# Kernel tuning notes

Hardware: AMD Instinct MI355X
Metric: run time of the kernel (lower is better)

Reference implementation:

```python
import jax, jax.numpy as jnp
import numpy as np

NEG_SLOPE = 0.2
LN_EPS = 1e-5


def _gat_layer(x, src, dst, W, a_src, a_dst, N):
    # x: [N, Fin], W: [Fin, H*C], a_src/a_dst: [H, C]
    H, C = a_src.shape
    h = (x @ W).reshape(N, H, C)
    al_src = (h * a_src).sum(-1)  # [N, H]
    al_dst = (h * a_dst).sum(-1)  # [N, H]
    e = jax.nn.leaky_relu(al_src[src] + al_dst[dst], NEG_SLOPE)  # [E, H]
    m = jax.ops.segment_max(e, dst, num_segments=N)
    e = jnp.exp(e - m[dst])
    denom = jax.ops.segment_sum(e, dst, num_segments=N)
    alpha = e / denom[dst]  # softmax over incoming edges per dst node
    msg = h[src] * alpha[:, :, None]  # [E, H, C]
    return jax.ops.segment_sum(msg, dst, num_segments=N)  # [N, H, C]


def _layer_norm(x, g, b):
    mu = x.mean(-1, keepdims=True)
    var = ((x - mu) ** 2).mean(-1, keepdims=True)
    return (x - mu) * jax.lax.rsqrt(var + LN_EPS) * g + b


def setup_inputs() -> dict:
    key = jax.random.key(0)
    ks = jax.random.split(key, 20)
    N, E, Fin, Ch, H = 50000, 800000, 128, 64, 4
    s = lambda k, shp, sc=0.05: jax.random.normal(k, shp, dtype=jnp.float32) * sc
    return {
        "x": jax.random.normal(ks[0], (N, Fin), dtype=jnp.float32),
        "edge_index": jax.random.randint(ks[1], (2, E), 0, N, dtype=jnp.int64),
        "W1": s(ks[2], (Fin, H * Ch)),
        "att_src1": s(ks[3], (H, Ch)),
        "att_dst1": s(ks[4], (H, Ch)),
        "b1": jnp.zeros((H * Ch,), jnp.float32),
        "ln1_g": jnp.ones((H * Ch,), jnp.float32),
        "ln1_b": jnp.zeros((H * Ch,), jnp.float32),
        "W2": s(ks[5], (H * Ch, Ch)),
        "att_src2": s(ks[6], (1, Ch)),
        "att_dst2": s(ks[7], (1, Ch)),
        "b2": jnp.zeros((Ch,), jnp.float32),
        "ln2_g": jnp.ones((Ch,), jnp.float32),
        "ln2_b": jnp.zeros((Ch,), jnp.float32),
        "fc1_W": s(ks[8], (Ch, Ch // 2)),
        "fc1_b": jnp.zeros((Ch // 2,), jnp.float32),
        "fc2_W": s(ks[9], (Ch // 2, 1)),
        "fc2_b": jnp.zeros((1,), jnp.float32),
    }


def reference(x, edge_index, W1, att_src1, att_dst1, b1, ln1_g, ln1_b,
              W2, att_src2, att_dst2, b2, ln2_g, ln2_b,
              fc1_W, fc1_b, fc2_W, fc2_b):
    N = x.shape[0]
    # PyG GATConv adds self-loops by default
    loop = jnp.arange(N, dtype=edge_index.dtype)
    src = jnp.concatenate([edge_index[0], loop])
    dst = jnp.concatenate([edge_index[1], loop])

    # GAT layer 1 (heads=4, concat) + LayerNorm + ReLU (dropout is identity in eval)
    h = _gat_layer(x, src, dst, W1, att_src1, att_dst1, N).reshape(N, -1) + b1
    h = jax.nn.relu(_layer_norm(h, ln1_g, ln1_b))

    # GAT layer 2 (heads=1) + LayerNorm + ReLU
    h = _gat_layer(h, src, dst, W2, att_src2, att_dst2, N).reshape(N, -1) + b2
    h = jax.nn.relu(_layer_norm(h, ln2_g, ln2_b))

    # MLP head
    h = jax.nn.relu(h @ fc1_W + fc1_b)
    return h @ fc2_W + fc2_b  # [N, 1]
```

## Files before the change

### kernel.cpp

```cpp
#include <hip/hip_runtime.h>
#include <hip/hip_fp16.h>
#include <math.h>

#define NEG_SLOPE 0.2f
#define LN_EPS 1e-5f

typedef __attribute__((ext_vector_type(8))) _Float16 half8;
typedef __attribute__((ext_vector_type(4))) _Float16 half4;
typedef __attribute__((ext_vector_type(4))) float floatx4;

static __device__ __forceinline__ float lrelu(float e) {
    return e > 0.0f ? e : NEG_SLOPE * e;
}

__global__ void k_zero(int* __restrict__ p, int n) {
    int i = blockIdx.x * blockDim.x + threadIdx.x;
    if (i < n) p[i] = 0;
}


__global__ __launch_bounds__(256) void k_bcount(
    const int* __restrict__ ei, int* __restrict__ gcount, int E, int N, int NB)
{
    __shared__ int hist[512];
    const int Et = E + N;
    for (int t = threadIdx.x; t < NB; t += 256) hist[t] = 0;
    __syncthreads();
    const int i0 = blockIdx.x * 8192;
#pragma unroll 4
    for (int j = 0; j < 32; ++j) {
        int i = i0 + j * 256 + threadIdx.x;
        if (i < Et) {
            int d = (i < E) ? ei[E + i] : (i - E);
            atomicAdd(&hist[d >> 7], 1);
        }
    }
    __syncthreads();
    for (int t = threadIdx.x; t < NB; t += 256)
        if (hist[t]) atomicAdd(&gcount[t], hist[t]);
}

__global__ __launch_bounds__(512) void k_bscan(
    const int* __restrict__ gcount, int* __restrict__ gbase, int* __restrict__ gcursor,
    int* __restrict__ offs, int NB, int N, int Et)
{
    __shared__ int ws[8];
    const int t = threadIdx.x, lane = t & 63, w = t >> 6;
    int v = (t < NB) ? gcount[t] : 0;
    int x = v;
#pragma unroll
    for (int o = 1; o < 64; o <<= 1) { int u = __shfl_up(x, o); if (lane >= o) x += u; }
    if (lane == 63) ws[w] = x;
    __syncthreads();
    if (t < 8) {
        int y = ws[t];
#pragma unroll
        for (int o = 1; o < 8; o <<= 1) { int u = __shfl_up(y, o); if (t >= o) y += u; }
        ws[t] = y;
    }
    __syncthreads();
    int excl = x - v + (w ? ws[w - 1] : 0);
    if (t < NB) { gbase[t] = excl; gcursor[t] = excl; }
    if (t == 0) offs[N] = Et;
}

__global__ __launch_bounds__(256) void k_bscatter(
    const int* __restrict__ ei, int* __restrict__ gcursor, int2* __restrict__ staged,
    int E, int N, int NB)
{
    __shared__ int hist[512];
    __shared__ int lbase[512];
    const int Et = E + N;
    for (int t = threadIdx.x; t < NB; t += 256) hist[t] = 0;
    __syncthreads();
    const int i0 = blockIdx.x * 8192;
#pragma unroll 4
    for (int j = 0; j < 32; ++j) {
        int i = i0 + j * 256 + threadIdx.x;
        if (i < Et) {
            int d = (i < E) ? ei[E + i] : (i - E);
            atomicAdd(&hist[d >> 7], 1);
        }
    }
    __syncthreads();
    for (int t = threadIdx.x; t < NB; t += 256) {
        int c = hist[t];
        lbase[t] = c ? atomicAdd(&gcursor[t], c) : 0;
    }
    __syncthreads();
    for (int t = threadIdx.x; t < NB; t += 256) hist[t] = 0;
    __syncthreads();
#pragma unroll 4
    for (int j = 0; j < 32; ++j) {
        int i = i0 + j * 256 + threadIdx.x;
        if (i < Et) {
            int s, d;
            if (i < E) { s = ei[i]; d = ei[E + i]; } else { s = d = i - E; }
            int b = d >> 7;
            int k = atomicAdd(&hist[b], 1);
            staged[lbase[b] + k] = make_int2(s, d);
        }
    }
}

__global__ __launch_bounds__(256) void k_bbuild(
    const int2* __restrict__ staged, const int* __restrict__ gcount, const int* __restrict__ gbase,
    int* __restrict__ offs, int* __restrict__ eidx, int N)
{
    __shared__ int ncnt[128];
    __shared__ int lcur[128];
    const int b = blockIdx.x;
    const int node0 = b << 7;
    const int base = gbase[b], cnt = gcount[b];
    for (int t = threadIdx.x; t < 128; t += 256) ncnt[t] = 0;
    __syncthreads();
    for (int t = threadIdx.x; t < cnt; t += 256)
        atomicAdd(&ncnt[staged[base + t].y - node0], 1);
    __syncthreads();
    if (threadIdx.x < 64) {
        const int lane = threadIdx.x;
        int a0 = ncnt[lane], a1 = ncnt[64 + lane];
        int x0 = a0, x1 = a1;
#pragma unroll
        for (int o = 1; o < 64; o <<= 1) {
            int t0 = __shfl_up(x0, o), t1 = __shfl_up(x1, o);
            if (lane >= o) { x0 += t0; x1 += t1; }
        }
        int tot0 = __shfl(x0, 63);
        int e0 = base + x0 - a0;
        int e1 = base + x1 - a1 + tot0;
        lcur[lane] = e0; lcur[64 + lane] = e1;
        int na = node0 + lane, nb = node0 + 64 + lane;
        if (na < N) offs[na] = e0;
        if (nb < N) offs[nb] = e1;
    }
    __syncthreads();
    for (int t = threadIdx.x; t < cnt; t += 256) {
        int2 sd = staged[base + t];
        int pos = atomicAdd(&lcur[sd.y - node0], 1);
        eidx[pos] = sd.x;
    }
}

__global__ __launch_bounds__(256) void k_gemm1(
    const float* __restrict__ x, const float* __restrict__ W1,
    const float* __restrict__ as1, const float* __restrict__ ad1,
    _Float16* __restrict__ h1, float* __restrict__ als, float* __restrict__ ald, int N)
{
    const int lane = threadIdx.x & 63, w = threadIdx.x >> 6;
    const int l15 = lane & 15, quad = lane >> 4;
    const int r_base = blockIdx.x * 64;

    half8 B[4][4];
    float asv[4], adv[4];
#pragma unroll
    for (int nt = 0; nt < 4; ++nt) {
        const int n = w * 64 + nt * 16 + l15;
        asv[nt] = as1[n]; adv[nt] = ad1[n];
#pragma unroll
        for (int ks = 0; ks < 4; ++ks) {
            const int k0 = ks * 32 + quad * 8;
            half8 b;
#pragma unroll
            for (int j = 0; j < 8; ++j) b[j] = (_Float16)W1[(size_t)(k0 + j) * 256 + n];
            B[ks][nt] = b;
        }
    }

#pragma unroll
    for (int rt = 0; rt < 4; ++rt) {
        const int r0 = r_base + rt * 16;
        int m = r0 + l15; if (m >= N) m = N - 1;
        half8 A[4];
#pragma unroll
        for (int ks = 0; ks < 4; ++ks) {
            const int k0 = ks * 32 + quad * 8;
            const float4* xp = (const float4*)(x + (size_t)m * 128 + k0);
            float4 v0 = xp[0], v1 = xp[1];
            half8 a;
            a[0] = (_Float16)v0.x; a[1] = (_Float16)v0.y; a[2] = (_Float16)v0.z; a[3] = (_Float16)v0.w;
            a[4] = (_Float16)v1.x; a[5] = (_Float16)v1.y; a[6] = (_Float16)v1.z; a[7] = (_Float16)v1.w;
            A[ks] = a;
        }
        floatx4 C[4];
#pragma unroll
        for (int nt = 0; nt < 4; ++nt) C[nt] = (floatx4){0.f, 0.f, 0.f, 0.f};
#pragma unroll
        for (int ks = 0; ks < 4; ++ks)
#pragma unroll
            for (int nt = 0; nt < 4; ++nt)
                C[nt] = __builtin_amdgcn_mfma_f32_16x16x32_f16(A[ks], B[ks][nt], C[nt], 0, 0, 0);

#pragma unroll
        for (int reg = 0; reg < 4; ++reg) {
            const int row = r0 + quad * 4 + reg;
            float vs = 0.f, vd = 0.f;
#pragma unroll
            for (int nt = 0; nt < 4; ++nt) {
                float c = C[nt][reg];
                if (row < N) h1[(size_t)row * 256 + w * 64 + nt * 16 + l15] = (_Float16)c;
                vs += c * asv[nt]; vd += c * adv[nt];
            }
#pragma unroll
            for (int o = 1; o < 16; o <<= 1) { vs += __shfl_xor(vs, o); vd += __shfl_xor(vd, o); }
            if (l15 == 0 && row < N) { als[row * 4 + w] = vs; ald[row * 4 + w] = vd; }
        }
    }
}

__global__ __launch_bounds__(256) void k_agg1(
    const _Float16* __restrict__ h1, const float* __restrict__ als, const float* __restrict__ ald,
    const int* __restrict__ offs, const int* __restrict__ eidx,
    const float* __restrict__ b1, const float* __restrict__ g1, const float* __restrict__ be1,
    _Float16* __restrict__ hln1, int N)
{
    const int wv = threadIdx.x >> 6, lane = threadIdx.x & 63;
    int n = blockIdx.x * 4 + wv;
    if (n >= N) n = N - 1;
    const int off0 = offs[n];
    const int deg = offs[n + 1] - off0;
    const float4 ad = ((const float4*)ald)[n];

    float m0 = -1e30f, m1 = -1e30f, m2 = -1e30f, m3 = -1e30f;
    float s0 = 0.f, s1 = 0.f, s2 = 0.f, s3 = 0.f;
    for (int j = lane; j < deg; j += 64) {
        int src = eidx[off0 + j];
        float4 a4 = ((const float4*)als)[src];
        float e, nm;
        e = lrelu(a4.x + ad.x); nm = fmaxf(m0, e); s0 = s0 * __expf(m0 - nm) + __expf(e - nm); m0 = nm;
        e = lrelu(a4.y + ad.y); nm = fmaxf(m1, e); s1 = s1 * __expf(m1 - nm) + __expf(e - nm); m1 = nm;
        e = lrelu(a4.z + ad.z); nm = fmaxf(m2, e); s2 = s2 * __expf(m2 - nm) + __expf(e - nm); m2 = nm;
        e = lrelu(a4.w + ad.w); nm = fmaxf(m3, e); s3 = s3 * __expf(m3 - nm) + __expf(e - nm); m3 = nm;
    }
#pragma unroll
    for (int o = 32; o; o >>= 1) {
        float mo, so, nm;
        mo = __shfl_xor(m0, o); so = __shfl_xor(s0, o);
        nm = fmaxf(m0, mo); s0 = s0 * __expf(m0 - nm) + so * __expf(mo - nm); m0 = nm;
        mo = __shfl_xor(m1, o); so = __shfl_xor(s1, o);
        nm = fmaxf(m1, mo); s1 = s1 * __expf(m1 - nm) + so * __expf(mo - nm); m1 = nm;
        mo = __shfl_xor(m2, o); so = __shfl_xor(s2, o);
        nm = fmaxf(m2, mo); s2 = s2 * __expf(m2 - nm) + so * __expf(mo - nm); m2 = nm;
        mo = __shfl_xor(m3, o); so = __shfl_xor(s3, o);
        nm = fmaxf(m3, mo); s3 = s3 * __expf(m3 - nm) + so * __expf(mo - nm); m3 = nm;
    }

    const int hd = lane >> 4, l15 = lane & 15;
    const float mh  = hd == 0 ? m0 : (hd == 1 ? m1 : (hd == 2 ? m2 : m3));
    const float sh_ = hd == 0 ? s0 : (hd == 1 ? s1 : (hd == 2 ? s2 : s3));
    const float adh = hd == 0 ? ad.x : (hd == 1 ? ad.y : (hd == 2 ? ad.z : ad.w));
    const float cc = -mh - __logf(sh_);

    float4 acc = make_float4(0.f, 0.f, 0.f, 0.f);
    const int bp_base = (lane & 48) << 2;
    for (int c0 = 0; c0 < deg; c0 += 16) {
        int nc = deg - c0; if (nc > 16) nc = 16;
        int j = c0 + l15; if (j >= deg) j = deg - 1;
        int srcv = eidx[off0 + j];
        float alpha = __expf(lrelu(als[srcv * 4 + hd] + adh) + cc);
        if (l15 >= nc) alpha = 0.f;
        for (int e0 = 0; e0 < nc; e0 += 4) {
#pragma unroll
            for (int u = 0; u < 4; ++u) {
                const int e = e0 + u;
                int s = __builtin_amdgcn_readlane(srcv, e);
                float a_e = __int_as_float(
                    __builtin_amdgcn_ds_bpermute(bp_base + e * 4, __float_as_int(alpha)));
                half4 v = *(const half4*)(h1 + (size_t)s * 256 + 4 * lane);
                acc.x = fmaf((float)v.x, a_e, acc.x);
                acc.y = fmaf((float)v.y, a_e, acc.y);
                acc.z = fmaf((float)v.z, a_e, acc.z);
                acc.w = fmaf((float)v.w, a_e, acc.w);
            }
        }
    }

    float4 bb = ((const float4*)b1)[lane];
    float y0 = acc.x + bb.x, y1 = acc.y + bb.y, y2 = acc.z + bb.z, y3 = acc.w + bb.w;
    float ps = y0 + y1 + y2 + y3;
    float pss = y0 * y0 + y1 * y1 + y2 * y2 + y3 * y3;
#pragma unroll
    for (int o = 32; o; o >>= 1) { ps += __shfl_xor(ps, o); pss += __shfl_xor(pss, o); }
    float mu = ps * (1.f / 256.f);
    float var = pss * (1.f / 256.f) - mu * mu;
    float rstd = rsqrtf(var + LN_EPS);
    float4 gg = ((const float4*)g1)[lane];
    float4 b2v = ((const float4*)be1)[lane];
    half4 outv;
    outv.x = (_Float16)fmaxf((y0 - mu) * rstd * gg.x + b2v.x, 0.f);
    outv.y = (_Float16)fmaxf((y1 - mu) * rstd * gg.y + b2v.y, 0.f);
    outv.z = (_Float16)fmaxf((y2 - mu) * rstd * gg.z + b2v.z, 0.f);
    outv.w = (_Float16)fmaxf((y3 - mu) * rstd * gg.w + b2v.w, 0.f);
    ((half4*)(hln1 + (size_t)n * 256))[lane] = outv;
}

__global__ __launch_bounds__(256) void k_gemm2(
    const _Float16* __restrict__ hln1, const float* __restrict__ W2,
    const float* __restrict__ as2, const float* __restrict__ ad2,
    _Float16* __restrict__ h2, float* __restrict__ als2, float* __restrict__ ald2, int N)
{
    __shared__ float ps_s[4][64], ps_d[4][64];
    const int lane = threadIdx.x & 63, w = threadIdx.x >> 6;
    const int l15 = lane & 15, quad = lane >> 4;
    const int r_base = blockIdx.x * 64;

    const int n = w * 16 + l15;
    const float asv = as2[n], adv = ad2[n];
    half8 B[8];
#pragma unroll
    for (int ks = 0; ks < 8; ++ks) {
        const int k0 = ks * 32 + quad * 8;
        half8 b;
#pragma unroll
        for (int j = 0; j < 8; ++j) b[j] = (_Float16)W2[(size_t)(k0 + j) * 64 + n];
        B[ks] = b;
    }

#pragma unroll
    for (int rt = 0; rt < 4; ++rt) {
        const int r0 = r_base + rt * 16;
        int m = r0 + l15; if (m >= N) m = N - 1;
        floatx4 C = (floatx4){0.f, 0.f, 0.f, 0.f};
#pragma unroll
        for (int ks = 0; ks < 8; ++ks) {
            half8 a = *(const half8*)(hln1 + (size_t)m * 256 + ks * 32 + quad * 8);
            C = __builtin_amdgcn_mfma_f32_16x16x32_f16(a, B[ks], C, 0, 0, 0);
        }
#pragma unroll
        for (int reg = 0; reg < 4; ++reg) {
            const int row = r0 + quad * 4 + reg;
            float c = C[reg];
            if (row < N) h2[(size_t)row * 64 + n] = (_Float16)c;
            float vs = c * asv, vd = c * adv;
#pragma unroll
            for (int o = 1; o < 16; o <<= 1) { vs += __shfl_xor(vs, o); vd += __shfl_xor(vd, o); }
            if (l15 == 0) {
                ps_s[w][rt * 16 + quad * 4 + reg] = vs;
                ps_d[w][rt * 16 + quad * 4 + reg] = vd;
            }
        }
    }
    __syncthreads();
    const int t = threadIdx.x;
    if (t < 64) {
        const int row = r_base + t;
        if (row < N) {
            als2[row] = ps_s[0][t] + ps_s[1][t] + ps_s[2][t] + ps_s[3][t];
            ald2[row] = ps_d[0][t] + ps_d[1][t] + ps_d[2][t] + ps_d[3][t];
        }
    }
}

__global__ __launch_bounds__(256) void k_agg2(
    const _Float16* __restrict__ h2, const float* __restrict__ als, const float* __restrict__ ald,
    const int* __restrict__ offs, const int* __restrict__ eidx,
    const float* __restrict__ b2, const float* __restrict__ g2, const float* __restrict__ be2,
    const float* __restrict__ fc1W, const float* __restrict__ fc1b,
    const float* __restrict__ fc2W, const float* __restrict__ fc2b,
    float* __restrict__ out, int N)
{
    __shared__ float sh[4][64];
    const int wv = threadIdx.x >> 6, lane = threadIdx.x & 63;
    int n = blockIdx.x * 4 + wv;
    if (n >= N) n = N - 1;
    const int off0 = offs[n];
    const int deg = offs[n + 1] - off0;
    const float adn = ald[n];

    float m = -1e30f, s = 0.f;
    for (int j = lane; j < deg; j += 64) {
        int src = eidx[off0 + j];
        float e = lrelu(als[src] + adn);
        float nm = fmaxf(m, e);
        s = s * __expf(m - nm) + __expf(e - nm); m = nm;
    }
#pragma unroll
    for (int o = 32; o; o >>= 1) {
        float mo = __shfl_xor(m, o), so = __shfl_xor(s, o);
        float nm = fmaxf(m, mo);
        s = s * __expf(m - nm) + so * __expf(mo - nm); m = nm;
    }
    const float cc = -m - __logf(s);

    float acc = 0.f;
    for (int c0 = 0; c0 < deg; c0 += 64) {
        int nc = deg - c0; if (nc > 64) nc = 64;
        int j = c0 + lane; if (j >= deg) j = deg - 1;
        int srcv = eidx[off0 + j];
        float alpha = __expf(lrelu(als[srcv] + adn) + cc);
        if (lane >= nc) alpha = 0.f;
        for (int e0 = 0; e0 < nc; e0 += 4) {
#pragma unroll
            for (int u = 0; u < 4; ++u) {
                const int e = e0 + u;
                int sidx = __builtin_amdgcn_readlane(srcv, e);
                float a_e = __int_as_float(
                    __builtin_amdgcn_readlane(__float_as_int(alpha), e));
                acc = fmaf((float)h2[(size_t)sidx * 64 + lane], a_e, acc);
            }
        }
    }

    float y = acc + b2[lane];
    float ps = y, pss = y * y;
#pragma unroll
    for (int o = 32; o; o >>= 1) { ps += __shfl_xor(ps, o); pss += __shfl_xor(pss, o); }
    float mu = ps * (1.f / 64.f);
    float var = pss * (1.f / 64.f) - mu * mu;
    float r = fmaxf((y - mu) * rsqrtf(var + LN_EPS) * g2[lane] + be2[lane], 0.f);

    sh[wv][lane] = r;
    __syncthreads();

    if (lane < 32) {
        float a1 = fc1b[lane];
#pragma unroll 8
        for (int k = 0; k < 64; ++k) a1 += sh[wv][k] * fc1W[k * 32 + lane];
        a1 = fmaxf(a1, 0.f);
        float t = a1 * fc2W[lane];
#pragma unroll
        for (int o = 16; o; o >>= 1) t += __shfl_xor(t, o);
        if (lane == 0) out[n] = t + fc2b[0];
    }
}

extern "C" void kernel_launch(void* const* d_in, const int* in_sizes, int n_in,
                              void* d_out, int out_size, void* d_ws, size_t ws_size,
                              hipStream_t stream)
{
    const float* x   = (const float*)d_in[0];
    const int* ei    = (const int*)d_in[1];
    const float* W1  = (const float*)d_in[2];
    const float* as1 = (const float*)d_in[3];
    const float* ad1 = (const float*)d_in[4];
    const float* b1  = (const float*)d_in[5];
    const float* g1  = (const float*)d_in[6];
    const float* be1 = (const float*)d_in[7];
    const float* W2  = (const float*)d_in[8];
    const float* as2 = (const float*)d_in[9];
    const float* ad2 = (const float*)d_in[10];
    const float* b2  = (const float*)d_in[11];
    const float* g2  = (const float*)d_in[12];
    const float* be2 = (const float*)d_in[13];
    const float* fc1W = (const float*)d_in[14];
    const float* fc1b = (const float*)d_in[15];
    const float* fc2W = (const float*)d_in[16];
    const float* fc2b = (const float*)d_in[17];
    float* out = (float*)d_out;

    const int N = in_sizes[0] / 128;
    const int E = in_sizes[1] / 2;
    const int Et = E + N;
    const int NB = (N + 127) >> 7;

    char* p = (char*)d_ws;
    auto carve = [&](size_t bytes) {
        void* q = p;
        p += (bytes + 255) & ~(size_t)255;
        return q;
    };
    _Float16* h1    = (_Float16*)carve((size_t)N * 256 * 2);
    _Float16* hln1h = (_Float16*)carve((size_t)N * 256 * 2);
    _Float16* h2    = (_Float16*)carve((size_t)N * 64 * 2);
    float* als1 = (float*)carve((size_t)N * 4 * 4);
    float* ald1 = (float*)carve((size_t)N * 4 * 4);
    float* als2 = (float*)carve((size_t)N * 4);
    float* ald2 = (float*)carve((size_t)N * 4);
    int* offs   = (int*)carve((size_t)(N + 1) * 4);
    int* eidx   = (int*)carve((size_t)Et * 4);
    int2* staged  = (int2*)carve((size_t)Et * 8);
    int* gcount  = (int*)carve(512 * 4);
    int* gbase   = (int*)carve(512 * 4);
    int* gcursor = (int*)carve(512 * 4);

    const int nchunks = (Et + 8191) / 8192;
    k_zero<<<(NB + 255) / 256, 256, 0, stream>>>(gcount, NB);
    k_bcount<<<nchunks, 256, 0, stream>>>(ei, gcount, E, N, NB);
    k_bscan<<<1, 512, 0, stream>>>(gcount, gbase, gcursor, offs, NB, N, Et);
    k_bscatter<<<nchunks, 256, 0, stream>>>(ei, gcursor, staged, E, N, NB);
    k_bbuild<<<NB, 256, 0, stream>>>(staged, gcount, gbase, offs, eidx, N);

    k_gemm1<<<(N + 63) / 64, 256, 0, stream>>>(x, W1, as1, ad1, h1, als1, ald1, N);
    k_agg1<<<(N + 3) / 4, 256, 0, stream>>>(h1, als1, ald1, offs, eidx, b1, g1, be1, hln1h, N);

    k_gemm2<<<(N + 63) / 64, 256, 0, stream>>>(hln1h, W2, as2, ad2, h2, als2, ald2, N);
    k_agg2<<<(N + 3) / 4, 256, 0, stream>>>(h2, als2, ald2, offs, eidx,
                                            b2, g2, be2, fc1W, fc1b, fc2W, fc2b, out, N);
}
```

Baseline: 313.8 us.

## Fuse bucket count into GEMM1 launch and process multiple edges per wave in aggregation

Merges the destination-bucket histogram kernel with the first GEMM into one launch, so the count blocks and GEMM tiles run concurrently, and drops the separate gemm1 launch. In agg1 each half-wave now handles a different edge with 8-wide fp16 loads, and the halves are combined with a cross-half shuffle. In agg2 four edges are processed in parallel per wave with 4-wide loads, and the per-edge count in bbuild is derived from adjacent gbase entries. This aims to increase memory-level parallelism in the gather loops, at the cost of extra shuffle reductions and more complex indexing.

```diff
diff --git a/kernel.cpp b/kernel.cpp
--- a/kernel.cpp
+++ b/kernel.cpp
@@ -4,6 +4,7 @@
 
 #define NEG_SLOPE 0.2f
 #define LN_EPS 1e-5f
+#define CHUNK 8192
 
 typedef __attribute__((ext_vector_type(8))) _Float16 half8;
 typedef __attribute__((ext_vector_type(4))) _Float16 half4;
@@ -18,138 +19,39 @@
     if (i < n) p[i] = 0;
 }
 
-
-__global__ __launch_bounds__(256) void k_bcount(
-    const int* __restrict__ ei, int* __restrict__ gcount, int E, int N, int NB)
-{
-    __shared__ int hist[512];
-    const int Et = E + N;
-    for (int t = threadIdx.x; t < NB; t += 256) hist[t] = 0;
-    __syncthreads();
-    const int i0 = blockIdx.x * 8192;
-#pragma unroll 4
-    for (int j = 0; j < 32; ++j) {
-        int i = i0 + j * 256 + threadIdx.x;
-        if (i < Et) {
-            int d = (i < E) ? ei[E + i] : (i - E);
-            atomicAdd(&hist[d >> 7], 1);
-        }
-    }
-    __syncthreads();
-    for (int t = threadIdx.x; t < NB; t += 256)
-        if (hist[t]) atomicAdd(&gcount[t], hist[t]);
-}
-
-__global__ __launch_bounds__(512) void k_bscan(
-    const int* __restrict__ gcount, int* __restrict__ gbase, int* __restrict__ gcursor,
-    int* __restrict__ offs, int NB, int N, int Et)
-{
-    __shared__ int ws[8];
-    const int t = threadIdx.x, lane = t & 63, w = t >> 6;
-    int v = (t < NB) ? gcount[t] : 0;
-    int x = v;
-#pragma unroll
-    for (int o = 1; o < 64; o <<= 1) { int u = __shfl_up(x, o); if (lane >= o) x += u; }
-    if (lane == 63) ws[w] = x;
-    __syncthreads();
-    if (t < 8) {
-        int y = ws[t];
-#pragma unroll
-        for (int o = 1; o < 8; o <<= 1) { int u = __shfl_up(y, o); if (t >= o) y += u; }
-        ws[t] = y;
-    }
-    __syncthreads();
-    int excl = x - v + (w ? ws[w - 1] : 0);
-    if (t < NB) { gbase[t] = excl; gcursor[t] = excl; }
-    if (t == 0) offs[N] = Et;
-}
-
-__global__ __launch_bounds__(256) void k_bscatter(
-    const int* __restrict__ ei, int* __restrict__ gcursor, int2* __restrict__ staged,
-    int E, int N, int NB)
-{
-    __shared__ int hist[512];
-    __shared__ int lbase[512];
-    const int Et = E + N;
-    for (int t = threadIdx.x; t < NB; t += 256) hist[t] = 0;
-    __syncthreads();
-    const int i0 = blockIdx.x * 8192;
-#pragma unroll 4
-    for (int j = 0; j < 32; ++j) {
-        int i = i0 + j * 256 + threadIdx.x;
-        if (i < Et) {
-            int d = (i < E) ? ei[E + i] : (i - E);
-            atomicAdd(&hist[d >> 7], 1);
-        }
-    }
-    __syncthreads();
-    for (int t = threadIdx.x; t < NB; t += 256) {
-        int c = hist[t];
-        lbase[t] = c ? atomicAdd(&gcursor[t], c) : 0;
-    }
-    __syncthreads();
-    for (int t = threadIdx.x; t < NB; t += 256) hist[t] = 0;
-    __syncthreads();
-#pragma unroll 4
-    for (int j = 0; j < 32; ++j) {
-        int i = i0 + j * 256 + threadIdx.x;
-        if (i < Et) {
-            int s, d;
-            if (i < E) { s = ei[i]; d = ei[E + i]; } else { s = d = i - E; }
-            int b = d >> 7;
-            int k = atomicAdd(&hist[b], 1);
-            staged[lbase[b] + k] = make_int2(s, d);
-        }
-    }
-}
-
-__global__ __launch_bounds__(256) void k_bbuild(
-    const int2* __restrict__ staged, const int* __restrict__ gcount, const int* __restrict__ gbase,
-    int* __restrict__ offs, int* __restrict__ eidx, int N)
-{
-    __shared__ int ncnt[128];
-    __shared__ int lcur[128];
-    const int b = blockIdx.x;
-    const int node0 = b << 7;
-    const int base = gbase[b], cnt = gcount[b];
-    for (int t = threadIdx.x; t < 128; t += 256) ncnt[t] = 0;
-    __syncthreads();
-    for (int t = threadIdx.x; t < cnt; t += 256)
-        atomicAdd(&ncnt[staged[base + t].y - node0], 1);
-    __syncthreads();
-    if (threadIdx.x < 64) {
-        const int lane = threadIdx.x;
-        int a0 = ncnt[lane], a1 = ncnt[64 + lane];
-        int x0 = a0, x1 = a1;
-#pragma unroll
-        for (int o = 1; o < 64; o <<= 1) {
-            int t0 = __shfl_up(x0, o), t1 = __shfl_up(x1, o);
-            if (lane >= o) { x0 += t0; x1 += t1; }
-        }
-        int tot0 = __shfl(x0, 63);
-        int e0 = base + x0 - a0;
-        int e1 = base + x1 - a1 + tot0;
-        lcur[lane] = e0; lcur[64 + lane] = e1;
-        int na = node0 + lane, nb = node0 + 64 + lane;
-        if (na < N) offs[na] = e0;
-        if (nb < N) offs[nb] = e1;
-    }
-    __syncthreads();
-    for (int t = threadIdx.x; t < cnt; t += 256) {
-        int2 sd = staged[base + t];
-        int pos = atomicAdd(&lcur[sd.y - node0], 1);
-        eidx[pos] = sd.x;
-    }
-}
-
-__global__ __launch_bounds__(256) void k_gemm1(
+__global__ __launch_bounds__(256) void k_g1bc(
     const float* __restrict__ x, const float* __restrict__ W1,
     const float* __restrict__ as1, const float* __restrict__ ad1,
-    _Float16* __restrict__ h1, float* __restrict__ als, float* __restrict__ ald, int N)
-{
-    const int lane = threadIdx.x & 63, w = threadIdx.x >> 6;
+    _Float16* __restrict__ h1, float* __restrict__ als, float* __restrict__ ald,
+    const int* __restrict__ ei, int* __restrict__ gcount,
+    int N, int E, int NB, int nchunks)
+{
+    __shared__ int hist[512];
+    const int tid = threadIdx.x;
+
+    if ((int)blockIdx.x < nchunks) {
+        const int Et = E + N;
+        for (int t = tid; t < NB; t += 256) hist[t] = 0;
+        __syncthreads();
+        const int i0 = blockIdx.x * CHUNK;
+#pragma unroll 4
+        for (int j = 0; j < CHUNK / 256; ++j) {
+            int i = i0 + j * 256 + tid;
+            if (i < Et) {
+                int d = (i < E) ? ei[E + i] : (i - E);
+                atomicAdd(&hist[d >> 7], 1);
+            }
+        }
+        __syncthreads();
+        for (int t = tid; t < NB; t += 256)
+            if (hist[t]) atomicAdd(&gcount[t], hist[t]);
+        return;
+    }
+
+    const int tile = blockIdx.x - nchunks;
+    const int lane = tid & 63, w = tid >> 6;
     const int l15 = lane & 15, quad = lane >> 4;
-    const int r_base = blockIdx.x * 64;
+    const int r_base = tile * 64;
 
     half8 B[4][4];
     float asv[4], adv[4];
@@ -205,6 +107,108 @@
             for (int o = 1; o < 16; o <<= 1) { vs += __shfl_xor(vs, o); vd += __shfl_xor(vd, o); }
             if (l15 == 0 && row < N) { als[row * 4 + w] = vs; ald[row * 4 + w] = vd; }
         }
+    }
+}
+
+__global__ __launch_bounds__(512) void k_bscan(
+    const int* __restrict__ gcount, int* __restrict__ gbase, int* __restrict__ gcursor,
+    int* __restrict__ offs, int NB, int N, int Et)
+{
+    __shared__ int ws[8];
+    const int t = threadIdx.x, lane = t & 63, w = t >> 6;
+    int v = (t < NB) ? gcount[t] : 0;
+    int x = v;
+#pragma unroll
+    for (int o = 1; o < 64; o <<= 1) { int u = __shfl_up(x, o); if (lane >= o) x += u; }
+    if (lane == 63) ws[w] = x;
+    __syncthreads();
+    if (t < 8) {
+        int y = ws[t];
+#pragma unroll
+        for (int o = 1; o < 8; o <<= 1) { int u = __shfl_up(y, o); if (t >= o) y += u; }
+        ws[t] = y;
+    }
+    __syncthreads();
+    int excl = x - v + (w ? ws[w - 1] : 0);
+    if (t < NB) { gbase[t] = excl; gcursor[t] = excl; }
+    if (t == 0) { offs[N] = Et; gbase[NB] = Et; }
+}
+
+__global__ __launch_bounds__(256) void k_bscatter(
+    const int* __restrict__ ei, int* __restrict__ gcursor, int2* __restrict__ staged,
+    int E, int N, int NB)
+{
+    __shared__ int hist[512];
+    __shared__ int lbase[512];
+    const int Et = E + N;
+    for (int t = threadIdx.x; t < NB; t += 256) hist[t] = 0;
+    __syncthreads();
+    const int i0 = blockIdx.x * CHUNK;
+#pragma unroll 4
+    for (int j = 0; j < CHUNK / 256; ++j) {
+        int i = i0 + j * 256 + threadIdx.x;
+        if (i < Et) {
+            int d = (i < E) ? ei[E + i] : (i - E);
+            atomicAdd(&hist[d >> 7], 1);
+        }
+    }
+    __syncthreads();
+    for (int t = threadIdx.x; t < NB; t += 256) {
+        int c = hist[t];
+        lbase[t] = c ? atomicAdd(&gcursor[t], c) : 0;
+    }
+    __syncthreads();
+    for (int t = threadIdx.x; t < NB; t += 256) hist[t] = 0;
+    __syncthreads();
+#pragma unroll 4
+    for (int j = 0; j < CHUNK / 256; ++j) {
+        int i = i0 + j * 256 + threadIdx.x;
+        if (i < Et) {
+            int s, d;
+            if (i < E) { s = ei[i]; d = ei[E + i]; } else { s = d = i - E; }
+            int b = d >> 7;
+            int k = atomicAdd(&hist[b], 1);
+            staged[lbase[b] + k] = make_int2(s, d);
+        }
+    }
+}
+
+__global__ __launch_bounds__(256) void k_bbuild(
+    const int2* __restrict__ staged, const int* __restrict__ gbase,
+    int* __restrict__ offs, int* __restrict__ eidx, int N)
+{
+    __shared__ int ncnt[128];
+    __shared__ int lcur[128];
+    const int b = blockIdx.x;
+    const int node0 = b << 7;
+    const int base = gbase[b], cnt = gbase[b + 1] - base;
+    for (int t = threadIdx.x; t < 128; t += 256) ncnt[t] = 0;
+    __syncthreads();
+    for (int t = threadIdx.x; t < cnt; t += 256)
+        atomicAdd(&ncnt[staged[base + t].y - node0], 1);
+    __syncthreads();
+    if (threadIdx.x < 64) {
+        const int lane = threadIdx.x;
+        int a0 = ncnt[lane], a1 = ncnt[64 + lane];
+        int x0 = a0, x1 = a1;
+#pragma unroll
+        for (int o = 1; o < 64; o <<= 1) {
+            int t0 = __shfl_up(x0, o), t1 = __shfl_up(x1, o);
+            if (lane >= o) { x0 += t0; x1 += t1; }
+        }
+        int tot0 = __shfl(x0, 63);
+        int e0 = base + x0 - a0;
+        int e1 = base + x1 - a1 + tot0;
+        lcur[lane] = e0; lcur[64 + lane] = e1;
+        int na = node0 + lane, nb = node0 + 64 + lane;
+        if (na < N) offs[na] = e0;
+        if (nb < N) offs[nb] = e1;
+    }
+    __syncthreads();
+    for (int t = threadIdx.x; t < cnt; t += 256) {
+        int2 sd = staged[base + t];
+        int pos = atomicAdd(&lcur[sd.y - node0], 1);
+        eidx[pos] = sd.x;
     }
 }
 
@@ -251,47 +255,62 @@
     const float adh = hd == 0 ? ad.x : (hd == 1 ? ad.y : (hd == 2 ? ad.z : ad.w));
     const float cc = -mh - __logf(sh_);
 
-    float4 acc = make_float4(0.f, 0.f, 0.f, 0.f);
-    const int bp_base = (lane & 48) << 2;
+    const int lane31 = lane & 31;
+    const int ehalf = lane >> 5;
+    const int hd2 = lane31 >> 3;
+    float accv[8];
+#pragma unroll
+    for (int j = 0; j < 8; ++j) accv[j] = 0.f;
+
     for (int c0 = 0; c0 < deg; c0 += 16) {
         int nc = deg - c0; if (nc > 16) nc = 16;
         int j = c0 + l15; if (j >= deg) j = deg - 1;
         int srcv = eidx[off0 + j];
         float alpha = __expf(lrelu(als[srcv * 4 + hd] + adh) + cc);
         if (l15 >= nc) alpha = 0.f;
-        for (int e0 = 0; e0 < nc; e0 += 4) {
-#pragma unroll
-            for (int u = 0; u < 4; ++u) {
-                const int e = e0 + u;
-                int s = __builtin_amdgcn_readlane(srcv, e);
-                float a_e = __int_as_float(
-                    __builtin_amdgcn_ds_bpermute(bp_base + e * 4, __float_as_int(alpha)));
-                half4 v = *(const half4*)(h1 + (size_t)s * 256 + 4 * lane);
-                acc.x = fmaf((float)v.x, a_e, acc.x);
-                acc.y = fmaf((float)v.y, a_e, acc.y);
-                acc.z = fmaf((float)v.z, a_e, acc.z);
-                acc.w = fmaf((float)v.w, a_e, acc.w);
-            }
-        }
-    }
-
-    float4 bb = ((const float4*)b1)[lane];
-    float y0 = acc.x + bb.x, y1 = acc.y + bb.y, y2 = acc.z + bb.z, y3 = acc.w + bb.w;
-    float ps = y0 + y1 + y2 + y3;
-    float pss = y0 * y0 + y1 * y1 + y2 * y2 + y3 * y3;
+        for (int e0 = 0; e0 < nc; e0 += 2) {
+            const int eLo = e0 + ehalf;
+            const int addr = (hd2 * 16 + (eLo & 15)) * 4;
+            float a_e = __int_as_float(
+                __builtin_amdgcn_ds_bpermute(addr, __float_as_int(alpha)));
+            int s_e = __builtin_amdgcn_ds_bpermute(addr, srcv);
+            const half8 v = *(const half8*)(h1 + (size_t)s_e * 256 + 8 * lane31);
+#pragma unroll
+            for (int q = 0; q < 8; ++q)
+                accv[q] = fmaf((float)v[q], a_e, accv[q]);
+        }
+    }
+#pragma unroll
+    for (int q = 0; q < 8; ++q) accv[q] += __shfl_xor(accv[q], 32);
+
+    const float4 bbA = ((const float4*)(b1 + 8 * lane31))[0];
+    const float4 bbB = ((const float4*)(b1 + 8 * lane31))[1];
+    float y[8];
+    y[0] = accv[0] + bbA.x; y[1] = accv[1] + bbA.y; y[2] = accv[2] + bbA.z; y[3] = accv[3] + bbA.w;
+    y[4] = accv[4] + bbB.x; y[5] = accv[5] + bbB.y; y[6] = accv[6] + bbB.z; y[7] = accv[7] + bbB.w;
+    float ps = 0.f, pss = 0.f;
+#pragma unroll
+    for (int q = 0; q < 8; ++q) { ps += y[q]; pss += y[q] * y[q]; }
 #pragma unroll
     for (int o = 32; o; o >>= 1) { ps += __shfl_xor(ps, o); pss += __shfl_xor(pss, o); }
-    float mu = ps * (1.f / 256.f);
-    float var = pss * (1.f / 256.f) - mu * mu;
+    float mu = ps * (1.f / 512.f);
+    float var = pss * (1.f / 512.f) - mu * mu;
     float rstd = rsqrtf(var + LN_EPS);
-    float4 gg = ((const float4*)g1)[lane];
-    float4 b2v = ((const float4*)be1)[lane];
-    half4 outv;
-    outv.x = (_Float16)fmaxf((y0 - mu) * rstd * gg.x + b2v.x, 0.f);
-    outv.y = (_Float16)fmaxf((y1 - mu) * rstd * gg.y + b2v.y, 0.f);
-    outv.z = (_Float16)fmaxf((y2 - mu) * rstd * gg.z + b2v.z, 0.f);
-    outv.w = (_Float16)fmaxf((y3 - mu) * rstd * gg.w + b2v.w, 0.f);
-    ((half4*)(hln1 + (size_t)n * 256))[lane] = outv;
+    const float4 ggA = ((const float4*)(g1 + 8 * lane31))[0];
+    const float4 ggB = ((const float4*)(g1 + 8 * lane31))[1];
+    const float4 beA = ((const float4*)(be1 + 8 * lane31))[0];
+    const float4 beB = ((const float4*)(be1 + 8 * lane31))[1];
+    half8 outv;
+    outv[0] = (_Float16)fmaxf((y[0] - mu) * rstd * ggA.x + beA.x, 0.f);
+    outv[1] = (_Float16)fmaxf((y[1] - mu) * rstd * ggA.y + beA.y, 0.f);
+    outv[2] = (_Float16)fmaxf((y[2] - mu) * rstd * ggA.z + beA.z, 0.f);
+    outv[3] = (_Float16)fmaxf((y[3] - mu) * rstd * ggA.w + beA.w, 0.f);
+    outv[4] = (_Float16)fmaxf((y[4] - mu) * rstd * ggB.x + beB.x, 0.f);
+    outv[5] = (_Float16)fmaxf((y[5] - mu) * rstd * ggB.y + beB.y, 0.f);
+    outv[6] = (_Float16)fmaxf((y[6] - mu) * rstd * ggB.z + beB.z, 0.f);
+    outv[7] = (_Float16)fmaxf((y[7] - mu) * rstd * ggB.w + beB.w, 0.f);
+    if (lane < 32)
+        *(half8*)(hln1 + (size_t)n * 256 + 8 * lane31) = outv;
 }
 
 __global__ __launch_bounds__(256) void k_gemm2(
@@ -382,7 +401,8 @@
     }
     const float cc = -m - __logf(s);
 
-    float acc = 0.f;
+    const int l15 = lane & 15, equad = lane >> 4;
+    float acc4[4] = {0.f, 0.f, 0.f, 0.f};
     for (int c0 = 0; c0 < deg; c0 += 64) {
         int nc = deg - c0; if (nc > 64) nc = 64;
         int j = c0 + lane; if (j >= deg) j = deg - 1;
@@ -390,27 +410,44 @@
         float alpha = __expf(lrelu(als[srcv] + adn) + cc);
         if (lane >= nc) alpha = 0.f;
         for (int e0 = 0; e0 < nc; e0 += 4) {
-#pragma unroll
-            for (int u = 0; u < 4; ++u) {
-                const int e = e0 + u;
-                int sidx = __builtin_amdgcn_readlane(srcv, e);
-                float a_e = __int_as_float(
-                    __builtin_amdgcn_readlane(__float_as_int(alpha), e));
-                acc = fmaf((float)h2[(size_t)sidx * 64 + lane], a_e, acc);
-            }
-        }
-    }
-
-    float y = acc + b2[lane];
-    float ps = y, pss = y * y;
+            const int eLo = (e0 + equad) & 63;
+            const int addr = eLo * 4;
+            float a_e = __int_as_float(
+                __builtin_amdgcn_ds_bpermute(addr, __float_as_int(alpha)));
+            int s_e = __builtin_amdgcn_ds_bpermute(addr, srcv);
+            const half4 v = *(const half4*)(h2 + (size_t)s_e * 64 + 4 * l15);
+#pragma unroll
+            for (int q = 0; q < 4; ++q)
+                acc4[q] = fmaf((float)v[q], a_e, acc4[q]);
+        }
+    }
+#pragma unroll
+    for (int q = 0; q < 4; ++q) {
+        acc4[q] += __shfl_xor(acc4[q], 16);
+        acc4[q] += __shfl_xor(acc4[q], 32);
+    }
+
+    const float4 bb = ((const float4*)(b2 + 4 * l15))[0];
+    float y[4];
+    y[0] = acc4[0] + bb.x; y[1] = acc4[1] + bb.y; y[2] = acc4[2] + bb.z; y[3] = acc4[3] + bb.w;
+    float ps = 0.f, pss = 0.f;
+#pragma unroll
+    for (int q = 0; q < 4; ++q) { ps += y[q]; pss += y[q] * y[q]; }
 #pragma unroll
     for (int o = 32; o; o >>= 1) { ps += __shfl_xor(ps, o); pss += __shfl_xor(pss, o); }
-    float mu = ps * (1.f / 64.f);
-    float var = pss * (1.f / 64.f) - mu * mu;
-    float r = fmaxf((y - mu) * rsqrtf(var + LN_EPS) * g2[lane] + be2[lane], 0.f);
-
-    sh[wv][lane] = r;
-    __syncthreads();
+    float mu = ps * (1.f / 256.f);
+    float var = pss * (1.f / 256.f) - mu * mu;
+    float rstd = rsqrtf(var + LN_EPS);
+    const float4 gg = ((const float4*)(g2 + 4 * l15))[0];
+    const float4 be = ((const float4*)(be2 + 4 * l15))[0];
+    float r0 = fmaxf((y[0] - mu) * rstd * gg.x + be.x, 0.f);
+    float r1 = fmaxf((y[1] - mu) * rstd * gg.y + be.y, 0.f);
+    float r2 = fmaxf((y[2] - mu) * rstd * gg.z + be.z, 0.f);
+    float r3 = fmaxf((y[3] - mu) * rstd * gg.w + be.w, 0.f);
+    if (equad == 0) {
+        sh[wv][4 * l15 + 0] = r0; sh[wv][4 * l15 + 1] = r1;
+        sh[wv][4 * l15 + 2] = r2; sh[wv][4 * l15 + 3] = r3;
+    }
 
     if (lane < 32) {
         float a1 = fc1b[lane];
@@ -452,6 +489,8 @@
     const int E = in_sizes[1] / 2;
     const int Et = E + N;
     const int NB = (N + 127) >> 7;
+    const int nchunks = (Et + CHUNK - 1) / CHUNK;
+    const int ntiles = (N + 63) / 64;
 
     char* p = (char*)d_ws;
     auto carve = [&](size_t bytes) {
@@ -468,19 +507,18 @@
     float* ald2 = (float*)carve((size_t)N * 4);
     int* offs   = (int*)carve((size_t)(N + 1) * 4);
     int* eidx   = (int*)carve((size_t)Et * 4);
-    int2* staged  = (int2*)carve((size_t)Et * 8);
+    int2* staged = (int2*)carve((size_t)Et * 8);
     int* gcount  = (int*)carve(512 * 4);
-    int* gbase   = (int*)carve(512 * 4);
+    int* gbase   = (int*)carve((512 + 1) * 4);
     int* gcursor = (int*)carve(512 * 4);
 
-    const int nchunks = (Et + 8191) / 8192;
     k_zero<<<(NB + 255) / 256, 256, 0, stream>>>(gcount, NB);
-    k_bcount<<<nchunks, 256, 0, stream>>>(ei, gcount, E, N, NB);
+    k_g1bc<<<nchunks + ntiles, 256, 0, stream>>>(x, W1, as1, ad1, h1, als1, ald1,
+                                                 ei, gcount, N, E, NB, nchunks);
     k_bscan<<<1, 512, 0, stream>>>(gcount, gbase, gcursor, offs, NB, N, Et);
     k_bscatter<<<nchunks, 256, 0, stream>>>(ei, gcursor, staged, E, N, NB);
-    k_bbuild<<<NB, 256, 0, stream>>>(staged, gcount, gbase, offs, eidx, N);
-
-    k_gemm1<<<(N + 63) / 64, 256, 0, stream>>>(x, W1, as1, ad1, h1, als1, ald1, N);
+    k_bbuild<<<NB, 256, 0, stream>>>(staged, gbase, offs, eidx, N);
+
     k_agg1<<<(N + 3) / 4, 256, 0, stream>>>(h1, als1, ald1, offs, eidx, b1, g1, be1, hln1h, N);
 
     k_gemm2<<<(N + 63) / 64, 256, 0, stream>>>(hln1h, W2, as2, ad2, h2, als2, ald2, N);
```

After: 314.4 us. About the same (+0.2%).
